# Kernel tuning notes

Hardware: AMD Instinct MI355X
Metric: run time of the kernel (lower is better)

Reference implementation:

```python
import jax, jax.numpy as jnp
import numpy as np

B, D, E, N = 2048, 4096, 512, 8192
BN_EPS = 1e-5
COS_EPS = 1e-8


def setup_inputs() -> dict:
    key = jax.random.key(0)
    k1, k2, k3, k4, k5 = jax.random.split(key, 5)
    vf = jax.random.normal(k1, (B, D), dtype=jnp.float32)
    p_wfs = jax.random.normal(k2, (B, D), dtype=jnp.float32)
    n_wfs = jax.random.normal(k3, (N, E), dtype=jnp.float32)
    # BatchNorm1d(4096) affine params (default init gamma=1, beta=0; use random-ish gamma for generality)
    gamma = jnp.ones((D,), dtype=jnp.float32)
    beta = jnp.zeros((D,), dtype=jnp.float32)
    # Linear(D -> E)
    lim = 1.0 / np.sqrt(D)
    W = jax.random.uniform(k4, (E, D), dtype=jnp.float32, minval=-lim, maxval=lim)
    b = jax.random.uniform(k5, (E,), dtype=jnp.float32, minval=-lim, maxval=lim)
    return {"vf": vf, "p_wfs": p_wfs, "n_wfs": n_wfs, "gamma": gamma, "beta": beta, "W": W, "b": b}


def _row_normalize(x, eps=COS_EPS):
    nrm = jnp.sqrt(jnp.sum(x * x, axis=-1, keepdims=True))
    return x / jnp.maximum(nrm, eps)


def reference(vf, p_wfs, n_wfs, gamma, beta, W, b):
    # BatchNorm1d in training mode: batch mean / biased variance over the batch dim
    mean = jnp.mean(vf, axis=0)
    var = jnp.mean((vf - mean) ** 2, axis=0)
    vfn = (vf - mean) * (gamma / jnp.sqrt(var + BN_EPS)) + beta  # [B, D]

    # Linear + ReLU embedding
    emb = jax.nn.relu(vfn @ W.T + b)  # [B, E]

    # p_e: row-wise cosine(normed vf, p_wfs) -> [B]
    p_e = jnp.sum(_row_normalize(vfn) * _row_normalize(p_wfs), axis=-1)

    # n_e: cosine(emb[v], n_wfs[n]) for all v,n -> one normalized GEMM [B, N]
    n_e = _row_normalize(emb) @ _row_normalize(n_wfs).T

    n_neg = n_wfs.shape[0]
    n_e_stack = n_e.reshape(-1, 1)                      # [B*N, 1]
    p_e_stack = jnp.repeat(p_e, n_neg).reshape(-1, 1)   # [B*N, 1], p_e[v] repeated N times
    return (n_e_stack, p_e_stack)
```

## Files before the change

kernel.cpp:

```cpp
#include <hip/hip_runtime.h>
#include <stdint.h>
#include <stddef.h>

#define B_ 2048
#define D_ 4096
#define E_ 512
#define N_ 8192
#define SPLITK 4

typedef unsigned short ushort_t;
typedef __attribute__((ext_vector_type(8))) short short8;
typedef __attribute__((ext_vector_type(4))) float floatx4;
typedef __attribute__((ext_vector_type(4))) unsigned short ushort4_t;

__device__ __forceinline__ void async_load16(const void* g, void* l) {
  __builtin_amdgcn_global_load_lds((__attribute__((address_space(1))) void*)(g),
                                   (__attribute__((address_space(3))) void*)(l), 16, 0, 0);
}

__device__ __forceinline__ ushort_t f2bf(float f) {
  unsigned int u = __float_as_uint(f);
  unsigned int r = (u + 0x7fffu + ((u >> 16) & 1u)) >> 16;
  return (ushort_t)r;
}
__device__ __forceinline__ float bf2f(ushort_t h) {
  return __uint_as_float(((unsigned int)h) << 16);
}

__global__ void bn_partial(const float* __restrict__ vf,
                           float* __restrict__ psum, float* __restrict__ psq) {
  int d = blockIdx.x * 256 + threadIdx.x;
  int chunk = blockIdx.y;
  float s = 0.f, q = 0.f;
  int r0 = chunk * 64;
  for (int r = r0; r < r0 + 64; ++r) {
    float v = vf[(size_t)r * D_ + d];
    s += v; q += v * v;
  }
  psum[chunk * D_ + d] = s;
  psq[chunk * D_ + d]  = q;
}

__global__ void bn_finalize(const float* __restrict__ psum, const float* __restrict__ psq,
                            const float* __restrict__ gamma, const float* __restrict__ beta,
                            float* __restrict__ scale, float* __restrict__ shift) {
  int d = blockIdx.x * 256 + threadIdx.x;
  float s = 0.f, q = 0.f;
  for (int c = 0; c < 32; ++c) { s += psum[c * D_ + d]; q += psq[c * D_ + d]; }
  float mean = s * (1.0f / B_);
  float var  = q * (1.0f / B_) - mean * mean;
  float sc = gamma[d] * rsqrtf(var + 1e-5f);
  scale[d] = sc;
  shift[d] = beta[d] - mean * sc;
}

__global__ __launch_bounds__(256) void pe_cast(const float* __restrict__ vf,
                                               const float* __restrict__ p,
                                               const float* __restrict__ scale,
                                               const float* __restrict__ shift,
                                               ushort_t* __restrict__ vfn,
                                               float* __restrict__ pe) {
  int v = blockIdx.x;
  const floatx4* vf4 = (const floatx4*)(vf + (size_t)v * D_);
  const floatx4* p4  = (const floatx4*)(p  + (size_t)v * D_);
  const floatx4* sc4 = (const floatx4*)scale;
  const floatx4* sh4 = (const floatx4*)shift;
  ushort_t* vrow = vfn + (size_t)v * D_;
  float sd = 0.f, sa = 0.f, sb = 0.f;
  for (int i = threadIdx.x; i < D_ / 4; i += 256) {
    floatx4 x = vf4[i], y = p4[i], s = sc4[i], t = sh4[i];
    ushort4_t o;
#pragma unroll
    for (int j = 0; j < 4; ++j) {
      float xn = x[j] * s[j] + t[j];
      o[j] = f2bf(xn);
      sd += xn * y[j]; sa += xn * xn; sb += y[j] * y[j];
    }
    *(ushort4_t*)(vrow + i * 4) = o;
  }
  for (int off = 32; off; off >>= 1) {
    sd += __shfl_down(sd, off); sa += __shfl_down(sa, off); sb += __shfl_down(sb, off);
  }
  __shared__ float red[3][4];
  int w = threadIdx.x >> 6, l = threadIdx.x & 63;
  if (l == 0) { red[0][w] = sd; red[1][w] = sa; red[2][w] = sb; }
  __syncthreads();
  if (threadIdx.x == 0) {
    sd = red[0][0] + red[0][1] + red[0][2] + red[0][3];
    sa = red[1][0] + red[1][1] + red[1][2] + red[1][3];
    sb = red[2][0] + red[2][1] + red[2][2] + red[2][3];
    float na = fmaxf(sqrtf(sa), 1e-8f), nb = fmaxf(sqrtf(sb), 1e-8f);
    pe[v] = sd / (na * nb);
  }
}

__global__ void cast_w(const float* __restrict__ W, ushort_t* __restrict__ out) {
  size_t i = ((size_t)blockIdx.x * 256 + threadIdx.x) * 4;
  floatx4 x = *(const floatx4*)(W + i);
  ushort4_t o;
#pragma unroll
  for (int j = 0; j < 4; ++j) o[j] = f2bf(x[j]);
  *(ushort4_t*)(out + i) = o;
}

__global__ void nw_kernel(const float* __restrict__ nw, ushort_t* __restrict__ nwb,
                          float* __restrict__ inv_nw) {
  int n = blockIdx.x;
  int t = threadIdx.x;
  floatx4 x = ((const floatx4*)(nw + (size_t)n * E_))[t];
  float s = x[0]*x[0] + x[1]*x[1] + x[2]*x[2] + x[3]*x[3];
  ushort4_t o;
#pragma unroll
  for (int j = 0; j < 4; ++j) o[j] = f2bf(x[j]);
  ((ushort4_t*)(nwb + (size_t)n * E_))[t] = o;
  for (int off = 32; off; off >>= 1) s += __shfl_down(s, off);
  __shared__ float r2[2];
  if ((t & 63) == 0) r2[t >> 6] = s;
  __syncthreads();
  if (t == 0) inv_nw[n] = 1.f / fmaxf(sqrtf(r2[0] + r2[1]), 1e-8f);
}

template <int BM, int BN, int BK, int WCOLS, int MT, int NT>
__device__ __forceinline__ void gemm_core(const ushort_t* __restrict__ A,
                                          const ushort_t* __restrict__ Bt, int K,
                                          int kb, int ke, int bm0, int bn0,
                                          ushort_t* As, ushort_t* Bs,
                                          floatx4 (&acc)[MT][NT]) {
  const int tid = threadIdx.x, w = tid >> 6, l = tid & 63;
  constexpr int ISS = BM * BK / 2048;
  const int wr = w / WCOLS, wc = w % WCOLS;
  const int m16 = l & 15, q = l >> 4;

  for (int k0 = kb; k0 < ke; k0 += BK) {
#pragma unroll
    for (int i = 0; i < ISS; ++i) {
      int e = i * 2048 + tid * 8;
      int row = e / BK, col = e % BK;
      async_load16(A + (size_t)(bm0 + row) * K + (k0 + col), &As[i * 2048 + w * 512]);
    }
#pragma unroll
    for (int i = 0; i < ISS; ++i) {
      int e = i * 2048 + tid * 8;
      int row = e / BK, col = e % BK;
      async_load16(Bt + (size_t)(bn0 + row) * K + (k0 + col), &Bs[i * 2048 + w * 512]);
    }
    __syncthreads();
#pragma unroll
    for (int kc = 0; kc < BK / 32; ++kc) {
      short8 af[MT], bf[NT];
#pragma unroll
      for (int i = 0; i < MT; ++i)
        af[i] = *(const short8*)&As[(wr * (MT * 16) + i * 16 + m16) * BK + kc * 32 + q * 8];
#pragma unroll
      for (int j = 0; j < NT; ++j)
        bf[j] = *(const short8*)&Bs[(wc * (NT * 16) + j * 16 + m16) * BK + kc * 32 + q * 8];
#pragma unroll
      for (int i = 0; i < MT; ++i)
#pragma unroll
        for (int j = 0; j < NT; ++j)
          acc[i][j] = __builtin_amdgcn_mfma_f32_16x16x32_bf16(af[i], bf[j], acc[i][j], 0, 0, 0);
    }
    __syncthreads();
  }
}

__global__ __launch_bounds__(256) void gemm1_splitk(const ushort_t* __restrict__ A,
                                                    const ushort_t* __restrict__ Bt,
                                                    float* __restrict__ partial) {
  __shared__ __align__(16) ushort_t As[64 * 64];
  __shared__ __align__(16) ushort_t Bs[64 * 64];
  floatx4 acc[2][2] = {};
  int bm0 = blockIdx.y * 64, bn0 = blockIdx.x * 64, s = blockIdx.z;
  int kb = s * (D_ / SPLITK);
  gemm_core<64, 64, 64, 2, 2, 2>(A, Bt, D_, kb, kb + D_ / SPLITK, bm0, bn0, As, Bs, acc);
  int tid = threadIdx.x, w = tid >> 6, l = tid & 63, m16 = l & 15, q = l >> 4;
  int wr = w >> 1, wc = w & 1;
  float* out = partial + (size_t)s * B_ * E_;
#pragma unroll
  for (int i = 0; i < 2; ++i)
#pragma unroll
    for (int j = 0; j < 2; ++j) {
      int col = bn0 + wc * 32 + j * 16 + m16;
#pragma unroll
      for (int r = 0; r < 4; ++r) {
        int row = bm0 + wr * 32 + i * 16 + q * 4 + r;
        out[(size_t)row * E_ + col] = acc[i][j][r];
      }
    }
}

__global__ __launch_bounds__(128) void gemm1_reduce(const float* __restrict__ partial,
                                                    const float* __restrict__ bias,
                                                    ushort_t* __restrict__ emb,
                                                    float* __restrict__ inv_emb) {
  int row = blockIdx.x, t = threadIdx.x;
  floatx4 v = {0.f, 0.f, 0.f, 0.f};
#pragma unroll
  for (int s = 0; s < SPLITK; ++s)
    v += *(const floatx4*)&partial[(size_t)s * B_ * E_ + (size_t)row * E_ + t * 4];
  floatx4 bb = *(const floatx4*)&bias[t * 4];
  ushort4_t o;
  float sumsq = 0.f;
#pragma unroll
  for (int j = 0; j < 4; ++j) {
    float f = fmaxf(v[j] + bb[j], 0.f);
    o[j] = f2bf(f);
    float fb = bf2f(o[j]);
    sumsq += fb * fb;
  }
  *(ushort4_t*)(emb + (size_t)row * E_ + t * 4) = o;
  for (int off = 32; off; off >>= 1) sumsq += __shfl_down(sumsq, off);
  __shared__ float r2[2];
  if ((t & 63) == 0) r2[t >> 6] = sumsq;
  __syncthreads();
  if (t == 0) inv_emb[row] = 1.f / fmaxf(sqrtf(r2[0] + r2[1]), 1e-8f);
}

__global__ __launch_bounds__(256) void gemm2_kernel(const ushort_t* __restrict__ A,
                                                    const ushort_t* __restrict__ Bt,
                                                    const float* __restrict__ inv_a,
                                                    const float* __restrict__ inv_b,
                                                    const float* __restrict__ pe,
                                                    float* __restrict__ out) {
  __shared__ __align__(16) ushort_t As[128 * 64];
  __shared__ __align__(16) ushort_t Bs[128 * 64];
  floatx4 acc[4][4] = {};
  int bm0 = blockIdx.y * 128, bn0 = blockIdx.x * 128;
  gemm_core<128, 128, 64, 2, 4, 4>(A, Bt, E_, 0, E_, bm0, bn0, As, Bs, acc);
  int tid = threadIdx.x, w = tid >> 6, l = tid & 63, m16 = l & 15, q = l >> 4;
  int wr = w >> 1, wc = w & 1;
  float* out2 = out + (size_t)B_ * N_;
  float ibv[4];
#pragma unroll
  for (int j = 0; j < 4; ++j) ibv[j] = inv_b[bn0 + wc * 64 + j * 16 + m16];
#pragma unroll
  for (int i = 0; i < 4; ++i)
#pragma unroll
    for (int r = 0; r < 4; ++r) {
      int row = bm0 + wr * 64 + i * 16 + q * 4 + r;
      float ia = inv_a[row];
      float pv = pe[row];
      size_t base = (size_t)row * N_ + bn0 + wc * 64 + m16;
#pragma unroll
      for (int j = 0; j < 4; ++j) {
        out[base + j * 16]  = acc[i][j][r] * ia * ibv[j];
        out2[base + j * 16] = pv;
      }
    }
}

extern "C" void kernel_launch(void* const* d_in, const int* in_sizes, int n_in,
                              void* d_out, int out_size, void* d_ws, size_t ws_size,
                              hipStream_t stream) {
  (void)in_sizes; (void)n_in; (void)out_size; (void)ws_size;
  const float* vf    = (const float*)d_in[0];
  const float* p_wfs = (const float*)d_in[1];
  const float* n_wfs = (const float*)d_in[2];
  const float* gamma = (const float*)d_in[3];
  const float* beta  = (const float*)d_in[4];
  const float* W     = (const float*)d_in[5];
  const float* bias  = (const float*)d_in[6];
  float* out = (float*)d_out;

  char* ws = (char*)d_ws;
  float* psum    = (float*)ws;  ws += (size_t)32 * D_ * 4;
  float* psq     = (float*)ws;  ws += (size_t)32 * D_ * 4;
  float* scale   = (float*)ws;  ws += (size_t)D_ * 4;
  float* shift   = (float*)ws;  ws += (size_t)D_ * 4;
  float* pe      = (float*)ws;  ws += (size_t)B_ * 4;
  float* inv_nw  = (float*)ws;  ws += (size_t)N_ * 4;
  float* inv_emb = (float*)ws;  ws += (size_t)B_ * 4;
  float* partial = (float*)ws;  ws += (size_t)SPLITK * B_ * E_ * 4;
  ushort_t* vfn  = (ushort_t*)ws;  ws += (size_t)B_ * D_ * 2;
  ushort_t* wb   = (ushort_t*)ws;  ws += (size_t)E_ * D_ * 2;
  ushort_t* nwb  = (ushort_t*)ws;  ws += (size_t)N_ * E_ * 2;
  ushort_t* emb  = (ushort_t*)ws;  ws += (size_t)B_ * E_ * 2;

  bn_partial<<<dim3(D_ / 256, 32), 256, 0, stream>>>(vf, psum, psq);
  bn_finalize<<<D_ / 256, 256, 0, stream>>>(psum, psq, gamma, beta, scale, shift);
  pe_cast<<<B_, 256, 0, stream>>>(vf, p_wfs, scale, shift, vfn, pe);
  cast_w<<<(E_ * D_ / 4) / 256, 256, 0, stream>>>(W, wb);
  nw_kernel<<<N_, 128, 0, stream>>>(n_wfs, nwb, inv_nw);
  gemm1_splitk<<<dim3(E_ / 64, B_ / 64, SPLITK), 256, 0, stream>>>(vfn, wb, partial);
  gemm1_reduce<<<B_, 128, 0, stream>>>(partial, bias, emb, inv_emb);
  gemm2_kernel<<<dim3(N_ / 128, B_ / 128), 256, 0, stream>>>(emb, nwb, inv_emb, inv_nw, pe, out);
}
```

Baseline: 283.6 us.

## Vectorize BN stats, use wave-per-row pe_cast, fuse prep casts, retile gemm1

The BN partial and finalize kernels now work on float4 columns, and the partial reduction is split into 64 row chunks. pe_cast now handles one row per wavefront, which removes the shared-memory block reduction and its barrier. The W cast and the n_wfs cast/norm kernels are merged into a single launch that uses wave-per-row for the norms. gemm1 moves to 128x64 tiles with split-K raised to 8, which improves per-block reuse but doubles the fp32 partial traffic that gemm1_reduce must read.

Result: slower. 293.8 us (+3.6%).

```diff
diff --git a/kernel.cpp b/kernel.cpp
--- a/kernel.cpp
+++ b/kernel.cpp
@@ -6,7 +6,7 @@
 #define D_ 4096
 #define E_ 512
 #define N_ 8192
-#define SPLITK 4
+#define SPLITK 8
 
 typedef unsigned short ushort_t;
 typedef __attribute__((ext_vector_type(8))) short short8;
@@ -27,31 +27,46 @@
   return __uint_as_float(((unsigned int)h) << 16);
 }
 
-__global__ void bn_partial(const float* __restrict__ vf,
-                           float* __restrict__ psum, float* __restrict__ psq) {
-  int d = blockIdx.x * 256 + threadIdx.x;
+__global__ __launch_bounds__(256) void bn_partial(const float* __restrict__ vf,
+                                                  float* __restrict__ psum,
+                                                  float* __restrict__ psq) {
+  int d4 = blockIdx.x * 256 + threadIdx.x;
   int chunk = blockIdx.y;
-  float s = 0.f, q = 0.f;
-  int r0 = chunk * 64;
-  for (int r = r0; r < r0 + 64; ++r) {
-    float v = vf[(size_t)r * D_ + d];
+  floatx4 s = {0.f, 0.f, 0.f, 0.f}, q = {0.f, 0.f, 0.f, 0.f};
+  int r0 = chunk * 32;
+  for (int r = r0; r < r0 + 32; ++r) {
+    floatx4 v = ((const floatx4*)(vf + (size_t)r * D_))[d4];
     s += v; q += v * v;
   }
-  psum[chunk * D_ + d] = s;
-  psq[chunk * D_ + d]  = q;
-}
-
-__global__ void bn_finalize(const float* __restrict__ psum, const float* __restrict__ psq,
-                            const float* __restrict__ gamma, const float* __restrict__ beta,
-                            float* __restrict__ scale, float* __restrict__ shift) {
-  int d = blockIdx.x * 256 + threadIdx.x;
-  float s = 0.f, q = 0.f;
-  for (int c = 0; c < 32; ++c) { s += psum[c * D_ + d]; q += psq[c * D_ + d]; }
-  float mean = s * (1.0f / B_);
-  float var  = q * (1.0f / B_) - mean * mean;
-  float sc = gamma[d] * rsqrtf(var + 1e-5f);
-  scale[d] = sc;
-  shift[d] = beta[d] - mean * sc;
+  ((floatx4*)(psum + (size_t)chunk * D_))[d4] = s;
+  ((floatx4*)(psq  + (size_t)chunk * D_))[d4] = q;
+}
+
+__global__ __launch_bounds__(256) void bn_finalize(const float* __restrict__ psum,
+                                                   const float* __restrict__ psq,
+                                                   const float* __restrict__ gamma,
+                                                   const float* __restrict__ beta,
+                                                   float* __restrict__ scale,
+                                                   float* __restrict__ shift) {
+  int d4 = blockIdx.x * 256 + threadIdx.x;
+  floatx4 s = {0.f, 0.f, 0.f, 0.f}, q = {0.f, 0.f, 0.f, 0.f};
+  for (int c = 0; c < 64; ++c) {
+    s += ((const floatx4*)(psum + (size_t)c * D_))[d4];
+    q += ((const floatx4*)(psq  + (size_t)c * D_))[d4];
+  }
+  floatx4 g = ((const floatx4*)gamma)[d4];
+  floatx4 bt = ((const floatx4*)beta)[d4];
+  floatx4 sc, sh;
+#pragma unroll
+  for (int j = 0; j < 4; ++j) {
+    float mean = s[j] * (1.0f / B_);
+    float var  = q[j] * (1.0f / B_) - mean * mean;
+    float scj  = g[j] * rsqrtf(var + 1e-5f);
+    sc[j] = scj;
+    sh[j] = bt[j] - mean * scj;
+  }
+  ((floatx4*)scale)[d4] = sc;
+  ((floatx4*)shift)[d4] = sh;
 }
 
 __global__ __launch_bounds__(256) void pe_cast(const float* __restrict__ vf,
@@ -60,14 +75,17 @@
                                                const float* __restrict__ shift,
                                                ushort_t* __restrict__ vfn,
                                                float* __restrict__ pe) {
-  int v = blockIdx.x;
+  int wv = threadIdx.x >> 6, l = threadIdx.x & 63;
+  int v = blockIdx.x * 4 + wv;
   const floatx4* vf4 = (const floatx4*)(vf + (size_t)v * D_);
   const floatx4* p4  = (const floatx4*)(p  + (size_t)v * D_);
   const floatx4* sc4 = (const floatx4*)scale;
   const floatx4* sh4 = (const floatx4*)shift;
   ushort_t* vrow = vfn + (size_t)v * D_;
   float sd = 0.f, sa = 0.f, sb = 0.f;
-  for (int i = threadIdx.x; i < D_ / 4; i += 256) {
+#pragma unroll 4
+  for (int k = 0; k < 16; ++k) {
+    int i = l + 64 * k;
     floatx4 x = vf4[i], y = p4[i], s = sc4[i], t = sh4[i];
     ushort4_t o;
 #pragma unroll
@@ -81,43 +99,42 @@
   for (int off = 32; off; off >>= 1) {
     sd += __shfl_down(sd, off); sa += __shfl_down(sa, off); sb += __shfl_down(sb, off);
   }
-  __shared__ float red[3][4];
-  int w = threadIdx.x >> 6, l = threadIdx.x & 63;
-  if (l == 0) { red[0][w] = sd; red[1][w] = sa; red[2][w] = sb; }
-  __syncthreads();
-  if (threadIdx.x == 0) {
-    sd = red[0][0] + red[0][1] + red[0][2] + red[0][3];
-    sa = red[1][0] + red[1][1] + red[1][2] + red[1][3];
-    sb = red[2][0] + red[2][1] + red[2][2] + red[2][3];
+  if (l == 0) {
     float na = fmaxf(sqrtf(sa), 1e-8f), nb = fmaxf(sqrtf(sb), 1e-8f);
     pe[v] = sd / (na * nb);
   }
 }
 
-__global__ void cast_w(const float* __restrict__ W, ushort_t* __restrict__ out) {
-  size_t i = ((size_t)blockIdx.x * 256 + threadIdx.x) * 4;
-  floatx4 x = *(const floatx4*)(W + i);
-  ushort4_t o;
-#pragma unroll
-  for (int j = 0; j < 4; ++j) o[j] = f2bf(x[j]);
-  *(ushort4_t*)(out + i) = o;
-}
-
-__global__ void nw_kernel(const float* __restrict__ nw, ushort_t* __restrict__ nwb,
-                          float* __restrict__ inv_nw) {
-  int n = blockIdx.x;
-  int t = threadIdx.x;
-  floatx4 x = ((const floatx4*)(nw + (size_t)n * E_))[t];
-  float s = x[0]*x[0] + x[1]*x[1] + x[2]*x[2] + x[3]*x[3];
-  ushort4_t o;
-#pragma unroll
-  for (int j = 0; j < 4; ++j) o[j] = f2bf(x[j]);
-  ((ushort4_t*)(nwb + (size_t)n * E_))[t] = o;
-  for (int off = 32; off; off >>= 1) s += __shfl_down(s, off);
-  __shared__ float r2[2];
-  if ((t & 63) == 0) r2[t >> 6] = s;
-  __syncthreads();
-  if (t == 0) inv_nw[n] = 1.f / fmaxf(sqrtf(r2[0] + r2[1]), 1e-8f);
+__global__ __launch_bounds__(256) void prep_kernel(const float* __restrict__ W,
+                                                   const float* __restrict__ nw,
+                                                   ushort_t* __restrict__ wb,
+                                                   ushort_t* __restrict__ nwb,
+                                                   float* __restrict__ inv_nw) {
+  int bid = blockIdx.x;
+  if (bid < 2048) {
+    size_t i = ((size_t)bid * 256 + threadIdx.x) * 4;
+    floatx4 x = *(const floatx4*)(W + i);
+    ushort4_t o;
+#pragma unroll
+    for (int j = 0; j < 4; ++j) o[j] = f2bf(x[j]);
+    *(ushort4_t*)(wb + i) = o;
+  } else {
+    int wv = threadIdx.x >> 6, l = threadIdx.x & 63;
+    int n = (bid - 2048) * 4 + wv;
+    const floatx4* src = (const floatx4*)(nw + (size_t)n * E_);
+    ushort4_t* dst = (ushort4_t*)(nwb + (size_t)n * E_);
+    float s = 0.f;
+#pragma unroll
+    for (int k = 0; k < 2; ++k) {
+      floatx4 x = src[l + 64 * k];
+      ushort4_t o;
+#pragma unroll
+      for (int j = 0; j < 4; ++j) { o[j] = f2bf(x[j]); s += x[j] * x[j]; }
+      dst[l + 64 * k] = o;
+    }
+    for (int off = 32; off; off >>= 1) s += __shfl_down(s, off);
+    if (l == 0) inv_nw[n] = 1.f / fmaxf(sqrtf(s), 1e-8f);
+  }
 }
 
 template <int BM, int BN, int BK, int WCOLS, int MT, int NT>
@@ -127,19 +144,20 @@
                                           ushort_t* As, ushort_t* Bs,
                                           floatx4 (&acc)[MT][NT]) {
   const int tid = threadIdx.x, w = tid >> 6, l = tid & 63;
-  constexpr int ISS = BM * BK / 2048;
+  constexpr int ISS_A = BM * BK / 2048;
+  constexpr int ISS_B = BN * BK / 2048;
   const int wr = w / WCOLS, wc = w % WCOLS;
   const int m16 = l & 15, q = l >> 4;
 
   for (int k0 = kb; k0 < ke; k0 += BK) {
 #pragma unroll
-    for (int i = 0; i < ISS; ++i) {
+    for (int i = 0; i < ISS_A; ++i) {
       int e = i * 2048 + tid * 8;
       int row = e / BK, col = e % BK;
       async_load16(A + (size_t)(bm0 + row) * K + (k0 + col), &As[i * 2048 + w * 512]);
     }
 #pragma unroll
-    for (int i = 0; i < ISS; ++i) {
+    for (int i = 0; i < ISS_B; ++i) {
       int e = i * 2048 + tid * 8;
       int row = e / BK, col = e % BK;
       async_load16(Bt + (size_t)(bn0 + row) * K + (k0 + col), &Bs[i * 2048 + w * 512]);
@@ -167,23 +185,23 @@
 __global__ __launch_bounds__(256) void gemm1_splitk(const ushort_t* __restrict__ A,
                                                     const ushort_t* __restrict__ Bt,
                                                     float* __restrict__ partial) {
-  __shared__ __align__(16) ushort_t As[64 * 64];
+  __shared__ __align__(16) ushort_t As[128 * 64];
   __shared__ __align__(16) ushort_t Bs[64 * 64];
-  floatx4 acc[2][2] = {};
-  int bm0 = blockIdx.y * 64, bn0 = blockIdx.x * 64, s = blockIdx.z;
+  floatx4 acc[4][2] = {};
+  int bm0 = blockIdx.y * 128, bn0 = blockIdx.x * 64, s = blockIdx.z;
   int kb = s * (D_ / SPLITK);
-  gemm_core<64, 64, 64, 2, 2, 2>(A, Bt, D_, kb, kb + D_ / SPLITK, bm0, bn0, As, Bs, acc);
+  gemm_core<128, 64, 64, 2, 4, 2>(A, Bt, D_, kb, kb + D_ / SPLITK, bm0, bn0, As, Bs, acc);
   int tid = threadIdx.x, w = tid >> 6, l = tid & 63, m16 = l & 15, q = l >> 4;
   int wr = w >> 1, wc = w & 1;
   float* out = partial + (size_t)s * B_ * E_;
 #pragma unroll
-  for (int i = 0; i < 2; ++i)
+  for (int i = 0; i < 4; ++i)
 #pragma unroll
     for (int j = 0; j < 2; ++j) {
       int col = bn0 + wc * 32 + j * 16 + m16;
 #pragma unroll
       for (int r = 0; r < 4; ++r) {
-        int row = bm0 + wr * 32 + i * 16 + q * 4 + r;
+        int row = bm0 + wr * 64 + i * 16 + q * 4 + r;
         out[(size_t)row * E_ + col] = acc[i][j][r];
       }
     }
@@ -263,8 +281,8 @@
   float* out = (float*)d_out;
 
   char* ws = (char*)d_ws;
-  float* psum    = (float*)ws;  ws += (size_t)32 * D_ * 4;
-  float* psq     = (float*)ws;  ws += (size_t)32 * D_ * 4;
+  float* psum    = (float*)ws;  ws += (size_t)64 * D_ * 4;
+  float* psq     = (float*)ws;  ws += (size_t)64 * D_ * 4;
   float* scale   = (float*)ws;  ws += (size_t)D_ * 4;
   float* shift   = (float*)ws;  ws += (size_t)D_ * 4;
   float* pe      = (float*)ws;  ws += (size_t)B_ * 4;
@@ -276,12 +294,11 @@
   ushort_t* nwb  = (ushort_t*)ws;  ws += (size_t)N_ * E_ * 2;
   ushort_t* emb  = (ushort_t*)ws;  ws += (size_t)B_ * E_ * 2;
 
-  bn_partial<<<dim3(D_ / 256, 32), 256, 0, stream>>>(vf, psum, psq);
-  bn_finalize<<<D_ / 256, 256, 0, stream>>>(psum, psq, gamma, beta, scale, shift);
-  pe_cast<<<B_, 256, 0, stream>>>(vf, p_wfs, scale, shift, vfn, pe);
-  cast_w<<<(E_ * D_ / 4) / 256, 256, 0, stream>>>(W, wb);
-  nw_kernel<<<N_, 128, 0, stream>>>(n_wfs, nwb, inv_nw);
-  gemm1_splitk<<<dim3(E_ / 64, B_ / 64, SPLITK), 256, 0, stream>>>(vfn, wb, partial);
+  bn_partial<<<dim3(D_ / 1024, 64), 256, 0, stream>>>(vf, psum, psq);
+  bn_finalize<<<D_ / 1024, 256, 0, stream>>>(psum, psq, gamma, beta, scale, shift);
+  pe_cast<<<B_ / 4, 256, 0, stream>>>(vf, p_wfs, scale, shift, vfn, pe);
+  prep_kernel<<<2048 + N_ / 4, 256, 0, stream>>>(W, n_wfs, wb, nwb, inv_nw);
+  gemm1_splitk<<<dim3(E_ / 64, B_ / 128, SPLITK), 256, 0, stream>>>(vfn, wb, partial);
   gemm1_reduce<<<B_, 128, 0, stream>>>(partial, bias, emb, inv_emb);
   gemm2_kernel<<<dim3(N_ / 128, B_ / 128), 256, 0, stream>>>(emb, nwb, inv_emb, inv_nw, pe, out);
 }
```
